# Kernel tuning notes

Hardware: AMD Instinct MI355X
Metric: run time of the kernel (lower is better)

The kernel has to match this reference:

```python
import jax, jax.numpy as jnp
import numpy as np

BN_EPS = 1e-5

def setup_inputs() -> dict:
    key = jax.random.key(0)
    ks = jax.random.split(key, 4)
    B, C, H, W = 8, 64, 128, 128
    return {
        "x": jax.random.normal(ks[0], (B, C, H, W), jnp.float32),
        "w_reduce": jax.random.normal(ks[1], (C, C), jnp.float32) * 0.05,
        "b_reduce": jnp.zeros((C,), jnp.float32),
        "bn_gamma": jnp.ones((C,), jnp.float32),
        "bn_beta": jnp.zeros((C,), jnp.float32),
        "w_span": jax.random.normal(ks[2], (9, C), jnp.float32) * 0.05,
        "b_span": jnp.zeros((9,), jnp.float32),
        "w_conv2": jax.random.normal(ks[3], (C, C, 3, 3), jnp.float32) * 0.02,
        "b_conv2": jnp.zeros((C,), jnp.float32),
    }


def _involution(x, w_reduce, b_reduce, bn_gamma, bn_beta, w_span, b_span):
    # Involution2d: in_ch == out_ch so initial_mapping is Identity; groups=1, reduce_ratio=1, stride=1.
    B, C, H, W = x.shape
    # unfold 3x3, pad 1 -> patches [B, C, 9, H, W] (torch unfold ordering: C major, then kh, kw)
    xp = jnp.pad(x, ((0, 0), (0, 0), (1, 1), (1, 1)))
    patches = jnp.stack(
        [xp[:, :, i:i + H, j:j + W] for i in range(3) for j in range(3)], axis=2
    )  # [B, C, 9, H, W]
    # kernel generation: 1x1 conv -> BatchNorm2d (batch stats) -> ReLU -> 1x1 conv
    r = jnp.einsum('oc,bchw->bohw', w_reduce, x) + b_reduce[None, :, None, None]
    mu = r.mean(axis=(0, 2, 3), keepdims=True)
    var = r.var(axis=(0, 2, 3), keepdims=True)
    rn = (r - mu) * jax.lax.rsqrt(var + BN_EPS)
    rn = jax.nn.relu(rn * bn_gamma[None, :, None, None] + bn_beta[None, :, None, None])
    kern = jnp.einsum('kc,bchw->bkhw', w_span, rn) + b_span[None, :, None, None]  # [B, 9, H, W]
    # per-pixel dynamic kernel applied to patches, summed over kernel axis
    return jnp.einsum('bkhw,bckhw->bchw', kern, patches)


def reference(x, w_reduce, b_reduce, bn_gamma, bn_beta, w_span, b_span, w_conv2, b_conv2):
    z = jax.nn.softplus(_involution(x, w_reduce, b_reduce, bn_gamma, bn_beta, w_span, b_span))
    y = jax.lax.conv_general_dilated(z, w_conv2, window_strides=(1, 1), padding=((1, 1), (1, 1)))
    y = y + b_conv2[None, :, None, None]
    return jax.nn.softplus(y)
```

## Files before the change

kernel.cpp:

```cpp
#include <hip/hip_runtime.h>
#include <math.h>

#define H_ 128
#define W_ 128
#define C_ 64
#define B_ 8
#define HW 16384
#define NPIX (B_*HW)

typedef __attribute__((ext_vector_type(8))) short short8;
typedef __attribute__((ext_vector_type(4))) float f32x4;

__device__ __forceinline__ float softplus_fast(float v) {
    return fmaxf(v, 0.f) + __logf(1.f + __expf(-fabsf(v)));
}

__device__ __forceinline__ unsigned short f2bf(float f) {
    unsigned u = __builtin_bit_cast(unsigned, f);
    unsigned r = (u + 0x7fffu + ((u >> 16) & 1u)) >> 16;
    return (unsigned short)r;
}

__device__ __forceinline__ void gl_lds16(const float* g, float* l) {
    __builtin_amdgcn_global_load_lds(
        (const __attribute__((address_space(1))) void*)g,
        (__attribute__((address_space(3))) void*)l, 16, 0, 0);
}

__global__ __launch_bounds__(256) void k0_wtr(const float* __restrict__ w2,
                                              const float* __restrict__ wr,
                                              const float* __restrict__ wspan,
                                              unsigned short* __restrict__ wtr,
                                              unsigned short* __restrict__ wtr1,
                                              unsigned short* __restrict__ wtr2)
{
    int t = blockIdx.x * 256 + threadIdx.x;
    if (t < 512) {
        int lane = t & 63, f = t >> 6;
        int mt = f >> 1, kh = f & 1;
        int o  = mt * 16 + (lane & 15);
        int c0 = kh * 32 + ((lane >> 4) << 3);
        uint4 pk;
        unsigned short* pv = (unsigned short*)&pk;
#pragma unroll
        for (int e = 0; e < 8; ++e)
            pv[e] = f2bf(wr[o * C_ + c0 + e]);
        *(uint4*)&wtr1[(size_t)t * 8] = pk;
    } else if (t < 640) {
        int tt = t - 512;
        int lane = tt & 63, kh = tt >> 6;
        int o  = lane & 15;
        int c0 = (kh << 5) + ((lane >> 4) << 3);
        uint4 pk;
        unsigned short* pv = (unsigned short*)&pk;
#pragma unroll
        for (int e = 0; e < 8; ++e)
            pv[e] = (o < 9) ? f2bf(wspan[o * C_ + c0 + e]) : (unsigned short)0;
        *(uint4*)&wtr2[(size_t)tt * 8] = pk;
    }
    if (t >= 4 * 18 * 64) return;
    int lane = t & 63;
    int f    = (t >> 6) % 18;
    int wv   = t / (18 * 64);
    int koff = f >> 1, ch = f & 1;
    int o = wv * 16 + (lane & 15);
    int cb = ch * 32 + ((lane >> 4) << 3);
    uint4 pk;
    unsigned short* pv = (unsigned short*)&pk;
#pragma unroll
    for (int e = 0; e < 8; ++e)
        pv[e] = f2bf(w2[(size_t)o * 576 + (size_t)(cb + e) * 9 + koff]);
    *(uint4*)&wtr[(size_t)t * 8] = pk;
}

__global__ __launch_bounds__(256) void k1_mfma(
    const float* __restrict__ x, const unsigned short* __restrict__ wtr1,
    const float* __restrict__ br, unsigned short* __restrict__ rb)
{
    __shared__ unsigned short xb[256 * 64];
    __shared__ float brs[C_];
    int tid = threadIdx.x;
    int blk = blockIdx.x;
    int pid0 = blk << 8;
    int b    = pid0 >> 14;
    int rem0 = pid0 & (HW - 1);
    const float* xbase = x + (((size_t)b * C_) << 14) + rem0;

    if (tid < C_) brs[tid] = br[tid];

    int p = tid;
#pragma unroll
    for (int m = 0; m < 8; ++m) {
        float tmp[8];
#pragma unroll
        for (int e = 0; e < 8; ++e)
            tmp[e] = xbase[((size_t)(m * 8 + e) << 14) + p];
        unsigned pk[4];
#pragma unroll
        for (int e = 0; e < 4; ++e)
            pk[e] = (unsigned)f2bf(tmp[2 * e]) | ((unsigned)f2bf(tmp[2 * e + 1]) << 16);
        *(uint4*)&xb[(p << 6) + ((m ^ (p & 7)) << 3)] = *(uint4*)pk;
    }

    int wid = tid >> 6, lane = tid & 63;
    int nl  = lane & 15;
    int kg  = lane >> 4;

    short8 af[8];
    const short8* wp = (const short8*)wtr1;
#pragma unroll
    for (int f = 0; f < 8; ++f) af[f] = wp[f * 64 + lane];

    f32x4 acc[4][4];
#pragma unroll
    for (int mt = 0; mt < 4; ++mt)
#pragma unroll
        for (int nt = 0; nt < 4; ++nt) acc[mt][nt] = (f32x4){0.f, 0.f, 0.f, 0.f};

    __syncthreads();

    int nbase = wid << 6;
#pragma unroll
    for (int nt = 0; nt < 4; ++nt) {
        int pp = nbase + (nt << 4) + nl;
#pragma unroll
        for (int kh = 0; kh < 2; ++kh) {
            int m = kh * 4 + kg;
            short8 bf = *(const short8*)&xb[(pp << 6) + ((m ^ (pp & 7)) << 3)];
#pragma unroll
            for (int mt = 0; mt < 4; ++mt)
                acc[mt][nt] = __builtin_amdgcn_mfma_f32_16x16x32_bf16(
                    af[mt * 2 + kh], bf, acc[mt][nt], 0, 0, 0);
        }
    }

    __syncthreads();

#pragma unroll
    for (int mt = 0; mt < 4; ++mt) {
        int c = (mt << 4) + (kg << 2);
        float b0 = brs[c], b1 = brs[c + 1], b2v = brs[c + 2], b3 = brs[c + 3];
        int chunk = c >> 3;
#pragma unroll
        for (int nt = 0; nt < 4; ++nt) {
            int pp = nbase + (nt << 4) + nl;
            f32x4 a = acc[mt][nt];
            unsigned lo = (unsigned)f2bf(a[0] + b0) | ((unsigned)f2bf(a[1] + b1) << 16);
            unsigned hi = (unsigned)f2bf(a[2] + b2v) | ((unsigned)f2bf(a[3] + b3) << 16);
            unsigned* dst = (unsigned*)&xb[(pp << 6) + ((chunk ^ (pp & 7)) << 3) + ((kg & 1) << 2)];
            dst[0] = lo;
            dst[1] = hi;
        }
    }
    __syncthreads();

    uint4* rp = (uint4*)(rb + ((size_t)(pid0 + p) << 6));
#pragma unroll
    for (int m = 0; m < 8; ++m)
        rp[m] = *(const uint4*)&xb[(p << 6) + ((m ^ (p & 7)) << 3)];
}

__global__ __launch_bounds__(256) void k1b_stats(
    const unsigned short* __restrict__ rb, float* __restrict__ stats)
{
    __shared__ float ls[128];
    int tid = threadIdx.x;
    if (tid < 128) ls[tid] = 0.f;
    __syncthreads();

    int j   = tid & 7;
    int row = (blockIdx.x << 5) + (tid >> 3);
    float s[8] = {0,0,0,0,0,0,0,0}, q[8] = {0,0,0,0,0,0,0,0};
    for (int p = row; p < NPIX; p += (gridDim.x << 5)) {
        uint4 v = *(const uint4*)(rb + ((size_t)p << 6) + (j << 3));
        const unsigned* u = (const unsigned*)&v;
#pragma unroll
        for (int e = 0; e < 4; ++e) {
            float lo = __builtin_bit_cast(float, u[e] << 16);
            float hi = __builtin_bit_cast(float, u[e] & 0xffff0000u);
            s[2*e]   += lo; q[2*e]   += lo * lo;
            s[2*e+1] += hi; q[2*e+1] += hi * hi;
        }
    }
#pragma unroll
    for (int e = 0; e < 8; ++e) {
#pragma unroll
        for (int m = 8; m <= 32; m <<= 1) {
            s[e] += __shfl_xor(s[e], m, 64);
            q[e] += __shfl_xor(q[e], m, 64);
        }
    }
    int lane = tid & 63;
    if (lane < 8) {
#pragma unroll
        for (int e = 0; e < 8; ++e) {
            atomicAdd(&ls[lane * 8 + e], s[e]);
            atomicAdd(&ls[64 + lane * 8 + e], q[e]);
        }
    }
    __syncthreads();
    if (tid < 128) atomicAdd(&stats[tid], ls[tid]);
}

__global__ __launch_bounds__(256) void k3_involution(
    const float* __restrict__ x, const unsigned short* __restrict__ rb,
    const float* __restrict__ stats, const float* __restrict__ gamma,
    const float* __restrict__ beta, const unsigned short* __restrict__ wtr2,
    const float* __restrict__ bspan, unsigned short* __restrict__ zb)
{
    __shared__ float xh0[3456], xh1[3456];
    __shared__ unsigned zs[256 * 32];
    __shared__ float a_s[C_], c_s[C_];

    int tid = threadIdx.x;
    if (tid < C_) {
        float inv_n = 1.f / (float)NPIX;
        float mu  = stats[tid] * inv_n;
        float var = stats[C_ + tid] * inv_n - mu * mu;
        float is  = rsqrtf(var + 1e-5f);
        float a   = gamma[tid] * is;
        a_s[tid] = a;
        c_s[tid] = beta[tid] - mu * a;
    }

    int blk = blockIdx.x;
    int b = blk >> 6, t = blk & 63;
    int h0 = (t >> 3) << 4, w0 = (t & 7) << 4;
    int ty = tid >> 4, tx = tid & 15;
    int pix = ((h0 + ty) << 7) + (w0 + tx);
    int pid = (b << 14) + pix;
    const float* xb_ = x + (((size_t)b * C_) << 14);
    const float* zgz = stats + 128;

    int goff[4];
#pragma unroll
    for (int k = 0; k < 4; ++k) {
        int item = (k << 8) + tid;
        int c    = item / 108;
        int rem  = item - c * 108;
        int row  = rem / 6;
        int ii   = rem - row * 6;
        int gh   = h0 + row - 1;
        int gw0  = w0 - 4 + (ii << 2);
        bool ok = (item < 864) && ((unsigned)gh < 128u) && ((unsigned)gw0 < 128u);
        goff[k] = ok ? ((c << 14) + (gh << 7) + gw0) : -1;
    }

    auto stage = [&](int g, float* buf) {
#pragma unroll
        for (int k = 0; k < 4; ++k) {
            if (k < 3 || tid < 96) {
                int item = (k << 8) + tid;
                const float* src = (goff[k] >= 0) ? (xb_ + (g << 17) + goff[k]) : zgz;
                gl_lds16(src, buf + (item << 2));
            }
        }
    };

    int lane = tid & 63;
    int w_  = tid >> 6;
    int nl  = lane & 15;
    int kg  = lane >> 4;
    short8 af0 = ((const short8*)wtr2)[lane];
    short8 af1 = ((const short8*)wtr2)[64 + lane];

    stage(0, xh0);
    __syncthreads();
    stage(1, xh1);

    float aa[2][8], cc[2][8];
#pragma unroll
    for (int kh = 0; kh < 2; ++kh) {
        int cb = (kh << 5) + (kg << 3);
#pragma unroll
        for (int e = 0; e < 8; ++e) { aa[kh][e] = a_s[cb + e]; cc[kh][e] = c_s[cb + e]; }
    }

    f32x4 acc9[4];
#pragma unroll
    for (int nt = 0; nt < 4; ++nt) acc9[nt] = (f32x4){0.f, 0.f, 0.f, 0.f};

#pragma unroll
    for (int nt = 0; nt < 4; ++nt) {
        int prow = h0 + (w_ << 2) + nt;
        int pid2 = (b << 14) + (prow << 7) + w0 + nl;
#pragma unroll
        for (int kh = 0; kh < 2; ++kh) {
            uint4 rv = *(const uint4*)(rb + ((size_t)pid2 << 6) + (kh << 5) + (kg << 3));
            const unsigned* ru = (const unsigned*)&rv;
            unsigned po[4];
#pragma unroll
            for (int e2 = 0; e2 < 4; ++e2) {
                float lo = __builtin_bit_cast(float, ru[e2] << 16);
                float hi = __builtin_bit_cast(float, ru[e2] & 0xffff0000u);
                float r0 = fmaxf(aa[kh][2 * e2]     * lo + cc[kh][2 * e2],     0.f);
                float r1 = fmaxf(aa[kh][2 * e2 + 1] * hi + cc[kh][2 * e2 + 1], 0.f);
                po[e2] = (unsigned)f2bf(r0) | ((unsigned)f2bf(r1) << 16);
            }
            short8 bfrag = __builtin_bit_cast(short8, *(uint4*)po);
            acc9[nt] = __builtin_amdgcn_mfma_f32_16x16x32_bf16(
                kh ? af1 : af0, bfrag, acc9[nt], 0, 0, 0);
        }
    }

    float* kl = (float*)zs;
#pragma unroll
    for (int nt = 0; nt < 4; ++nt) {
        int px = (w_ << 6) + (nt << 4) + nl;
#pragma unroll
        for (int e = 0; e < 4; ++e) {
            int rr = (kg << 2) + e;
            if (rr < 9) kl[px * 9 + rr] = acc9[nt][e];
        }
    }
    __syncthreads();
    float kern[9];
#pragma unroll
    for (int k = 0; k < 9; ++k) kern[k] = kl[tid * 9 + k] + bspan[k];
    __syncthreads();

#pragma unroll 1
    for (int g = 0; g < 8; ++g) {
        if (g >= 1 && g < 7) stage(g + 1, (g & 1) ? xh0 : xh1);
        const float* xf = (g & 1) ? xh1 : xh0;
        unsigned pk[4];
#pragma unroll
        for (int cp = 0; cp < 4; ++cp) {
            const float* p0 = xf + (cp * 2) * 432 + ty * 24 + tx + 3;
            const float* p1 = p0 + 432;
            float acc0 = 0.f, acc1 = 0.f;
#pragma unroll
            for (int i = 0; i < 3; ++i)
#pragma unroll
                for (int j = 0; j < 3; ++j) {
                    float kv = kern[i * 3 + j];
                    acc0 += kv * p0[i * 24 + j];
                    acc1 += kv * p1[i * 24 + j];
                }
            pk[cp] = (unsigned)f2bf(softplus_fast(acc0))
                   | ((unsigned)f2bf(softplus_fast(acc1)) << 16);
        }
        *(uint4*)&zs[(tid << 5) + ((g ^ (tid & 7)) << 2)] = *(uint4*)pk;
        if (g < 7) __syncthreads();
    }

    uint4* zp = (uint4*)(zb + ((size_t)pid << 6));
#pragma unroll
    for (int k = 0; k < 8; ++k)
        zp[k] = *(const uint4*)&zs[(tid << 5) + ((k ^ (tid & 7)) << 2)];
}

__global__ __launch_bounds__(256) void k4_mfma(
    const unsigned short* __restrict__ zb, const unsigned short* __restrict__ wtr,
    const float* __restrict__ b2, float* __restrict__ out)
{
    __shared__ unsigned short zt[324 * 64];
    int tid = threadIdx.x;
    int blk = blockIdx.x;
    int b = blk >> 6;
    int t = blk & 63;
    int h0 = (t >> 3) << 4;
    int w0 = (t & 7) << 4;

    for (int idx = tid; idx < 324 * 8; idx += 256) {
        int p  = idx >> 3;
        int cg = idx & 7;
        int py = p / 18, px = p - py * 18;
        int gh = h0 + py - 1, gw = w0 + px - 1;
        uint4 v = make_uint4(0u, 0u, 0u, 0u);
        if ((unsigned)gh < 128u && (unsigned)gw < 128u)
            v = *(const uint4*)(zb + (((size_t)((b << 14) + (gh << 7) + gw)) << 6) + (cg << 3));
        *(uint4*)&zt[(p << 6) + ((cg ^ (p & 7)) << 3)] = v;
    }

    int wid  = tid >> 6, lane = tid & 63;
    int nl   = lane & 15;
    int kg   = lane >> 4;

    short8 wf[18];
    const short8* wp = (const short8*)wtr;
#pragma unroll
    for (int f = 0; f < 18; ++f)
        wf[f] = wp[(size_t)(wid * 18 + f) * 64 + lane];

    f32x4 acc[16];
#pragma unroll
    for (int nt = 0; nt < 16; ++nt) acc[nt] = (f32x4){0.f, 0.f, 0.f, 0.f};

    __syncthreads();

#pragma unroll
    for (int y = 0; y < 18; ++y) {
        short8 bf[6];
#pragma unroll
        for (int j = 0; j < 3; ++j)
#pragma unroll
            for (int ch = 0; ch < 2; ++ch) {
                int p  = y * 18 + j + nl;
                int cg = ch * 4 + kg;
                bf[j * 2 + ch] = *(const short8*)&zt[(p << 6) + ((cg ^ (p & 7)) << 3)];
            }
#pragma unroll
        for (int i = 0; i < 3; ++i) {
            int nt = y - i;
            if (nt >= 0 && nt < 16) {
#pragma unroll
                for (int j = 0; j < 3; ++j)
#pragma unroll
                    for (int ch = 0; ch < 2; ++ch)
                        acc[nt] = __builtin_amdgcn_mfma_f32_16x16x32_bf16(
                            wf[(i * 3 + j) * 2 + ch], bf[j * 2 + ch], acc[nt], 0, 0, 0);
            }
        }
    }

    float bias[4];
#pragma unroll
    for (int r = 0; r < 4; ++r) bias[r] = b2[(wid << 4) + (kg << 2) + r];

    size_t ob = ((size_t)b) << 20;
#pragma unroll
    for (int nt = 0; nt < 16; ++nt) {
        int h = h0 + nt;
#pragma unroll
        for (int r = 0; r < 4; ++r) {
            int o = (wid << 4) + (kg << 2) + r;
            float v = acc[nt][r] + bias[r];
            out[ob + ((size_t)o << 14) + (h << 7) + w0 + nl] = softplus_fast(v);
        }
    }
}

extern "C" void kernel_launch(void* const* d_in, const int* in_sizes, int n_in,
                              void* d_out, int out_size, void* d_ws, size_t ws_size,
                              hipStream_t stream)
{
    const float* x   = (const float*)d_in[0];
    const float* wr  = (const float*)d_in[1];
    const float* br  = (const float*)d_in[2];
    const float* gam = (const float*)d_in[3];
    const float* bet = (const float*)d_in[4];
    const float* wsp = (const float*)d_in[5];
    const float* bsp = (const float*)d_in[6];
    const float* w2  = (const float*)d_in[7];
    const float* b2  = (const float*)d_in[8];
    float* out = (float*)d_out;

    unsigned short* zb   = (unsigned short*)d_ws;
    unsigned short* wtr  = zb + (size_t)NPIX * C_;
    unsigned short* wtr1 = wtr + 4608 * 8;
    unsigned short* wtr2 = wtr1 + 512 * 8;
    float* stats = (float*)(wtr2 + 128 * 8);

    unsigned short* rb = (unsigned short*)d_out;

    hipMemsetAsync(stats, 0, 1024, stream);
    k0_wtr<<<18, 256, 0, stream>>>(w2, wr, wsp, wtr, wtr1, wtr2);
    k1_mfma<<<NPIX / 256, 256, 0, stream>>>(x, wtr1, br, rb);
    k1b_stats<<<128, 256, 0, stream>>>(rb, stats);
    k3_involution<<<NPIX / 256, 256, 0, stream>>>(x, rb, stats, gam, bet, wtr2, bsp, zb);
    k4_mfma<<<NPIX / 256, 256, 0, stream>>>(zb, wtr, b2, out);
}
```

Baseline: 87.71 us.

## Fuse BatchNorm statistics reduction into the reduce-conv MFMA kernel

Computes per-channel sum and sum-of-squares in the epilogue of the 1x1 reduce MFMA kernel, reduced with wave shuffles, shared-memory atomics and one global atomic per channel per block. This removes the separate stats kernel that re-read the whole bf16 intermediate. The stats zeroing also moves into the weight-prep kernel, which drops a memset launch. Statistics are now taken from fp32 values before bf16 rounding, which shifts numerics slightly, and the reduce kernel gains register pressure plus many global atomics from its 512 blocks.

```diff
diff --git a/kernel.cpp b/kernel.cpp
--- a/kernel.cpp
+++ b/kernel.cpp
@@ -32,9 +32,11 @@
                                               const float* __restrict__ wspan,
                                               unsigned short* __restrict__ wtr,
                                               unsigned short* __restrict__ wtr1,
-                                              unsigned short* __restrict__ wtr2)
+                                              unsigned short* __restrict__ wtr2,
+                                              float* __restrict__ stats)
 {
     int t = blockIdx.x * 256 + threadIdx.x;
+    if (t < 256) stats[t] = 0.f;
     if (t < 512) {
         int lane = t & 63, f = t >> 6;
         int mt = f >> 1, kh = f & 1;
@@ -75,10 +77,12 @@
 
 __global__ __launch_bounds__(256) void k1_mfma(
     const float* __restrict__ x, const unsigned short* __restrict__ wtr1,
-    const float* __restrict__ br, unsigned short* __restrict__ rb)
+    const float* __restrict__ br, unsigned short* __restrict__ rb,
+    float* __restrict__ stats)
 {
     __shared__ unsigned short xb[256 * 64];
     __shared__ float brs[C_];
+    __shared__ float ls[128];
     int tid = threadIdx.x;
     int blk = blockIdx.x;
     int pid0 = blk << 8;
@@ -87,6 +91,7 @@
     const float* xbase = x + (((size_t)b * C_) << 14) + rem0;
 
     if (tid < C_) brs[tid] = br[tid];
+    if (tid < 128) ls[tid] = 0.f;
 
     int p = tid;
 #pragma unroll
@@ -135,6 +140,10 @@
     }
 
     __syncthreads();
+
+    float s_[16], q_[16];
+#pragma unroll
+    for (int i = 0; i < 16; ++i) { s_[i] = 0.f; q_[i] = 0.f; }
 
 #pragma unroll
     for (int mt = 0; mt < 4; ++mt) {
@@ -145,61 +154,42 @@
         for (int nt = 0; nt < 4; ++nt) {
             int pp = nbase + (nt << 4) + nl;
             f32x4 a = acc[mt][nt];
-            unsigned lo = (unsigned)f2bf(a[0] + b0) | ((unsigned)f2bf(a[1] + b1) << 16);
-            unsigned hi = (unsigned)f2bf(a[2] + b2v) | ((unsigned)f2bf(a[3] + b3) << 16);
+            float v0 = a[0] + b0, v1 = a[1] + b1, v2 = a[2] + b2v, v3 = a[3] + b3;
+            s_[mt * 4 + 0] += v0; q_[mt * 4 + 0] += v0 * v0;
+            s_[mt * 4 + 1] += v1; q_[mt * 4 + 1] += v1 * v1;
+            s_[mt * 4 + 2] += v2; q_[mt * 4 + 2] += v2 * v2;
+            s_[mt * 4 + 3] += v3; q_[mt * 4 + 3] += v3 * v3;
+            unsigned lo = (unsigned)f2bf(v0) | ((unsigned)f2bf(v1) << 16);
+            unsigned hi = (unsigned)f2bf(v2) | ((unsigned)f2bf(v3) << 16);
             unsigned* dst = (unsigned*)&xb[(pp << 6) + ((chunk ^ (pp & 7)) << 3) + ((kg & 1) << 2)];
             dst[0] = lo;
             dst[1] = hi;
         }
     }
-    __syncthreads();
+
+#pragma unroll
+    for (int i = 0; i < 16; ++i) {
+#pragma unroll
+        for (int m = 1; m <= 8; m <<= 1) {
+            s_[i] += __shfl_xor(s_[i], m, 64);
+            q_[i] += __shfl_xor(q_[i], m, 64);
+        }
+    }
+    if (nl == 0) {
+#pragma unroll
+        for (int i = 0; i < 16; ++i) {
+            int c = ((i >> 2) << 4) + (kg << 2) + (i & 3);
+            atomicAdd(&ls[c], s_[i]);
+            atomicAdd(&ls[64 + c], q_[i]);
+        }
+    }
+    __syncthreads();
+    if (tid < 128) atomicAdd(&stats[tid], ls[tid]);
 
     uint4* rp = (uint4*)(rb + ((size_t)(pid0 + p) << 6));
 #pragma unroll
     for (int m = 0; m < 8; ++m)
         rp[m] = *(const uint4*)&xb[(p << 6) + ((m ^ (p & 7)) << 3)];
-}
-
-__global__ __launch_bounds__(256) void k1b_stats(
-    const unsigned short* __restrict__ rb, float* __restrict__ stats)
-{
-    __shared__ float ls[128];
-    int tid = threadIdx.x;
-    if (tid < 128) ls[tid] = 0.f;
-    __syncthreads();
-
-    int j   = tid & 7;
-    int row = (blockIdx.x << 5) + (tid >> 3);
-    float s[8] = {0,0,0,0,0,0,0,0}, q[8] = {0,0,0,0,0,0,0,0};
-    for (int p = row; p < NPIX; p += (gridDim.x << 5)) {
-        uint4 v = *(const uint4*)(rb + ((size_t)p << 6) + (j << 3));
-        const unsigned* u = (const unsigned*)&v;
-#pragma unroll
-        for (int e = 0; e < 4; ++e) {
-            float lo = __builtin_bit_cast(float, u[e] << 16);
-            float hi = __builtin_bit_cast(float, u[e] & 0xffff0000u);
-            s[2*e]   += lo; q[2*e]   += lo * lo;
-            s[2*e+1] += hi; q[2*e+1] += hi * hi;
-        }
-    }
-#pragma unroll
-    for (int e = 0; e < 8; ++e) {
-#pragma unroll
-        for (int m = 8; m <= 32; m <<= 1) {
-            s[e] += __shfl_xor(s[e], m, 64);
-            q[e] += __shfl_xor(q[e], m, 64);
-        }
-    }
-    int lane = tid & 63;
-    if (lane < 8) {
-#pragma unroll
-        for (int e = 0; e < 8; ++e) {
-            atomicAdd(&ls[lane * 8 + e], s[e]);
-            atomicAdd(&ls[64 + lane * 8 + e], q[e]);
-        }
-    }
-    __syncthreads();
-    if (tid < 128) atomicAdd(&stats[tid], ls[tid]);
 }
 
 __global__ __launch_bounds__(256) void k3_involution(
@@ -454,10 +444,8 @@
 
     unsigned short* rb = (unsigned short*)d_out;
 
-    hipMemsetAsync(stats, 0, 1024, stream);
-    k0_wtr<<<18, 256, 0, stream>>>(w2, wr, wsp, wtr, wtr1, wtr2);
-    k1_mfma<<<NPIX / 256, 256, 0, stream>>>(x, wtr1, br, rb);
-    k1b_stats<<<128, 256, 0, stream>>>(rb, stats);
+    k0_wtr<<<18, 256, 0, stream>>>(w2, wr, wsp, wtr, wtr1, wtr2, stats);
+    k1_mfma<<<NPIX / 256, 256, 0, stream>>>(x, wtr1, br, rb, stats);
     k3_involution<<<NPIX / 256, 256, 0, stream>>>(x, rb, stats, gam, bet, wtr2, bsp, zb);
     k4_mfma<<<NPIX / 256, 256, 0, stream>>>(zb, wtr, b2, out);
 }
```

New measurement: 80.84 us. -7.8%, faster.
